# Optimization experiments

Measured on AMD Instinct MI355X. Metric: run time of the kernel, lower is better.

## Reference

```python
import jax, jax.numpy as jnp
import numpy as np

FEATURE_DIM = 64
HIDDEN = 128

def _xavier(key, shape):
    fan_in, fan_out = shape
    limit = float(np.sqrt(6.0 / (fan_in + fan_out)))
    return jax.random.uniform(key, shape, jnp.float32, -limit, limit)

def setup_inputs() -> dict:
    key = jax.random.key(0)
    ks = jax.random.split(key, 12)
    x = jax.random.normal(ks[0], (64, 4096, FEATURE_DIM), jnp.float32)
    h_t = jax.random.normal(ks[1], (64 * 4096, HIDDEN), jnp.float32)
    c_t = jax.random.normal(ks[2], (64 * 4096, HIDDEN), jnp.float32)
    W_xi = _xavier(ks[3], (FEATURE_DIM, HIDDEN)); W_hi = _xavier(ks[4], (HIDDEN, HIDDEN))
    W_xf = _xavier(ks[5], (FEATURE_DIM, HIDDEN)); W_hf = _xavier(ks[6], (HIDDEN, HIDDEN))
    W_xc = _xavier(ks[7], (FEATURE_DIM, HIDDEN)); W_hc = _xavier(ks[8], (HIDDEN, HIDDEN))
    W_xo = _xavier(ks[9], (FEATURE_DIM, HIDDEN)); W_ho = _xavier(ks[10], (HIDDEN, HIDDEN))
    b_i = jnp.zeros((HIDDEN,), jnp.float32)
    b_f = jnp.zeros((HIDDEN,), jnp.float32)
    b_c = jnp.zeros((HIDDEN,), jnp.float32)
    b_o = jnp.zeros((HIDDEN,), jnp.float32)
    return {"x": x, "h_t": h_t, "c_t": c_t,
            "W_xi": W_xi, "W_hi": W_hi, "b_i": b_i,
            "W_xf": W_xf, "W_hf": W_hf, "b_f": b_f,
            "W_xc": W_xc, "W_hc": W_hc, "b_c": b_c,
            "W_xo": W_xo, "W_ho": W_ho, "b_o": b_o}

def reference(x, h_t, c_t, W_xi, W_hi, b_i, W_xf, W_hf, b_f, W_xc, W_hc, b_c, W_xo, W_ho, b_o):
    bs, num_nodes, feature_dim = x.shape
    xf = x.reshape(bs * num_nodes, feature_dim)  # [N, F]
    # Fused form: concatenate the 4 gate weights -> 2 GEMMs + one elementwise pass
    Wx = jnp.concatenate([W_xi, W_xf, W_xc, W_xo], axis=1)   # [F, 4H]
    Wh = jnp.concatenate([W_hi, W_hf, W_hc, W_ho], axis=1)   # [H, 4H]
    b = jnp.concatenate([b_i, b_f, b_c, b_o])                # [4H]
    gates = xf @ Wx + h_t @ Wh + b                           # [N, 4H]
    H = h_t.shape[1]
    i_t = jax.nn.sigmoid(gates[:, 0 * H:1 * H])
    f_t = jax.nn.sigmoid(gates[:, 1 * H:2 * H])
    c_hat = jnp.tanh(gates[:, 2 * H:3 * H])
    o_t = jax.nn.sigmoid(gates[:, 3 * H:4 * H])
    c_new = f_t * c_t + i_t * c_hat
    h_new = o_t * jnp.tanh(c_new)
    return (h_new, c_new)
```

## Files before the change

### kernel.cpp

```cpp
#include <hip/hip_runtime.h>
#include <hip/hip_bf16.h>


#define N_ROWS (64 * 4096)
#define HDIM 128
#define FDIM 64
#define KDIM 192
#define NKS 12
#define M_TILE 32

typedef __bf16 bf16_t;
typedef __bf16 bf16x8 __attribute__((ext_vector_type(8)));
typedef float f32x16 __attribute__((ext_vector_type(16)));

__global__ void swizzle_weights(const float* __restrict__ Wxi, const float* __restrict__ Whi,
                                const float* __restrict__ Wxf, const float* __restrict__ Whf,
                                const float* __restrict__ Wxc, const float* __restrict__ Whc,
                                const float* __restrict__ Wxo, const float* __restrict__ Who,
                                bf16_t* __restrict__ Bsw) {
    int gid = blockIdx.x * 256 + threadIdx.x;
    int l  = gid & 63;
    int ct = (gid >> 6) & 15;
    int ks = gid >> 10;
    int kb = ks * 16 + (l >> 5) * 8;
    int n  = ct * 32 + (l & 31);
    int g  = n >> 7;
    int c  = n & 127;
    const float* Wx = (g == 0) ? Wxi : (g == 1) ? Wxf : (g == 2) ? Wxc : Wxo;
    const float* Wh = (g == 0) ? Whi : (g == 1) ? Whf : (g == 2) ? Whc : Who;
    bf16x8 v;
#pragma unroll
    for (int j = 0; j < 8; ++j) {
        int k = kb + j;
        float f = (k < FDIM) ? Wx[k * HDIM + c] : Wh[(k - FDIM) * HDIM + c];
        v[j] = (bf16_t)f;
    }
    *(bf16x8*)(Bsw + (long)gid * 8) = v;
}

__device__ inline float fast_rcp(float x) { return __builtin_amdgcn_rcpf(x); }
__device__ inline float sigm(float x) {
    x = fminf(fmaxf(x, -30.f), 30.f);
    return fast_rcp(1.f + __expf(-x));
}
__device__ inline float tanh_f(float x) {
    x = fminf(fmaxf(x, -15.f), 15.f);
    float e = __expf(-2.f * x);
    return (1.f - e) * fast_rcp(1.f + e);
}

__global__ __launch_bounds__(256, 3)
void lstm_fused(const float* __restrict__ x, const float* __restrict__ h_t,
                const float* __restrict__ c_t,
                const float* __restrict__ b_i, const float* __restrict__ b_f,
                const float* __restrict__ b_c, const float* __restrict__ b_o,
                const bf16_t* __restrict__ Bsw,
                float* __restrict__ h_out, float* __restrict__ c_out) {
    const int tid  = threadIdx.x;
    const int wave = tid >> 6;
    const int lane = tid & 63;
    const long row_base = (long)blockIdx.x * M_TILE;

    const int arow = lane & 31;
    const int ksl  = (lane >> 5) * 8;
    const float* ax = x   + (row_base + arow) * FDIM + ksl;
    const float* ah = h_t + (row_base + arow) * HDIM + ksl;

    const int col   = wave * 32 + (lane & 31);
    const int rhalf = 4 * (lane >> 5);

    float cpre[16];
#pragma unroll
    for (int r = 0; r < 16; ++r) {
        int row_l = (r & 3) + 8 * (r >> 2) + rhalf;
        cpre[r] = c_t[(row_base + row_l) * HDIM + col];
    }
    const float bi = b_i[col], bf = b_f[col], bc = b_c[col], bo = b_o[col];

    f32x16 acc0 = {}, acc1 = {}, acc2 = {}, acc3 = {};
    const bf16_t* b_base = Bsw + wave * 512 + (long)lane * 8;

#pragma unroll
    for (int ks = 0; ks < NKS; ++ks) {
        const float* ap = (ks < 4) ? (ax + ks * 16) : (ah + (ks - 4) * 16);
        float4 f0 = *(const float4*)(ap);
        float4 f1 = *(const float4*)(ap + 4);
        bf16x8 a;
        a[0] = (bf16_t)f0.x; a[1] = (bf16_t)f0.y; a[2] = (bf16_t)f0.z; a[3] = (bf16_t)f0.w;
        a[4] = (bf16_t)f1.x; a[5] = (bf16_t)f1.y; a[6] = (bf16_t)f1.z; a[7] = (bf16_t)f1.w;

        const bf16_t* bp = b_base + (long)ks * 8192;
        bf16x8 b0 = *(const bf16x8*)(bp);
        bf16x8 b1 = *(const bf16x8*)(bp + 2048);
        bf16x8 b2 = *(const bf16x8*)(bp + 4096);
        bf16x8 b3 = *(const bf16x8*)(bp + 6144);
        acc0 = __builtin_amdgcn_mfma_f32_32x32x16_bf16(a, b0, acc0, 0, 0, 0);
        acc1 = __builtin_amdgcn_mfma_f32_32x32x16_bf16(a, b1, acc1, 0, 0, 0);
        acc2 = __builtin_amdgcn_mfma_f32_32x32x16_bf16(a, b2, acc2, 0, 0, 0);
        acc3 = __builtin_amdgcn_mfma_f32_32x32x16_bf16(a, b3, acc3, 0, 0, 0);
    }

#pragma unroll
    for (int r = 0; r < 16; ++r) {
        int row_l = (r & 3) + 8 * (r >> 2) + rhalf;
        long idx = (row_base + row_l) * HDIM + col;
        float gi = acc0[r] + bi;
        float gf = acc1[r] + bf;
        float gc = acc2[r] + bc;
        float go = acc3[r] + bo;
        float i_t = sigm(gi);
        float f_t = sigm(gf);
        float ch  = tanh_f(gc);
        float o_t = sigm(go);
        float cn = f_t * cpre[r] + i_t * ch;
        float hn = o_t * tanh_f(cn);
        h_out[idx] = hn;
        c_out[idx] = cn;
    }
}

extern "C" void kernel_launch(void* const* d_in, const int* in_sizes, int n_in,
                              void* d_out, int out_size, void* d_ws, size_t ws_size,
                              hipStream_t stream) {
    const float* x    = (const float*)d_in[0];
    const float* h_t  = (const float*)d_in[1];
    const float* c_t  = (const float*)d_in[2];
    const float* W_xi = (const float*)d_in[3];
    const float* W_hi = (const float*)d_in[4];
    const float* b_i  = (const float*)d_in[5];
    const float* W_xf = (const float*)d_in[6];
    const float* W_hf = (const float*)d_in[7];
    const float* b_f  = (const float*)d_in[8];
    const float* W_xc = (const float*)d_in[9];
    const float* W_hc = (const float*)d_in[10];
    const float* b_c  = (const float*)d_in[11];
    const float* W_xo = (const float*)d_in[12];
    const float* W_ho = (const float*)d_in[13];
    const float* b_o  = (const float*)d_in[14];

    bf16_t* Bsw = (bf16_t*)d_ws;
    float* h_out = (float*)d_out;
    float* c_out = h_out + (long)N_ROWS * HDIM;

    swizzle_weights<<<48, 256, 0, stream>>>(W_xi, W_hi, W_xf, W_hf,
                                            W_xc, W_hc, W_xo, W_ho, Bsw);
    lstm_fused<<<N_ROWS / M_TILE, 256, 0, stream>>>(x, h_t, c_t, b_i, b_f, b_c, b_o,
                                                    Bsw, h_out, c_out);
}
```

Baseline: 616.0 us.

## Retile LSTM kernel by row block and gate column, staging weights in LDS

```diff
diff --git a/kernel.cpp b/kernel.cpp
--- a/kernel.cpp
+++ b/kernel.cpp
@@ -7,7 +7,8 @@
 #define FDIM 64
 #define KDIM 192
 #define NKS 12
-#define M_TILE 32
+#define RBLK 128
+#define PH_KS 6
 
 typedef __bf16 bf16_t;
 typedef __bf16 bf16x8 __attribute__((ext_vector_type(8)));
@@ -49,61 +50,85 @@
     return (1.f - e) * fast_rcp(1.f + e);
 }
 
-__global__ __launch_bounds__(256, 3)
+__global__ __launch_bounds__(256, 4)
 void lstm_fused(const float* __restrict__ x, const float* __restrict__ h_t,
                 const float* __restrict__ c_t,
                 const float* __restrict__ b_i, const float* __restrict__ b_f,
                 const float* __restrict__ b_c, const float* __restrict__ b_o,
                 const bf16_t* __restrict__ Bsw,
                 float* __restrict__ h_out, float* __restrict__ c_out) {
+    __shared__ bf16_t bsh[PH_KS * 4 * 512];
+
     const int tid  = threadIdx.x;
     const int wave = tid >> 6;
     const int lane = tid & 63;
-    const long row_base = (long)blockIdx.x * M_TILE;
 
-    const int arow = lane & 31;
-    const int ksl  = (lane >> 5) * 8;
-    const float* ax = x   + (row_base + arow) * FDIM + ksl;
-    const float* ah = h_t + (row_base + arow) * HDIM + ksl;
+    const int bid     = blockIdx.x;
+    const int logical = ((bid & 7) << 10) | (bid >> 3);
+    const int c_blk   = logical & 3;
+    const long row_base = (long)(logical >> 2) * RBLK;
 
-    const int col   = wave * 32 + (lane & 31);
+    const int r0  = wave * 32 + (lane & 31);
+    const int ksl = (lane >> 5) * 8;
+    const float* ax = x   + (row_base + r0) * FDIM + ksl;
+    const float* ah = h_t + (row_base + r0) * HDIM + ksl;
+
+    const int col   = c_blk * 32 + (lane & 31);
     const int rhalf = 4 * (lane >> 5);
+    const int wrow  = wave * 32;
 
     float cpre[16];
 #pragma unroll
     for (int r = 0; r < 16; ++r) {
         int row_l = (r & 3) + 8 * (r >> 2) + rhalf;
-        cpre[r] = c_t[(row_base + row_l) * HDIM + col];
+        cpre[r] = c_t[(row_base + wrow + row_l) * HDIM + col];
     }
     const float bi = b_i[col], bf = b_f[col], bc = b_c[col], bo = b_o[col];
 
     f32x16 acc0 = {}, acc1 = {}, acc2 = {}, acc3 = {};
-    const bf16_t* b_base = Bsw + wave * 512 + (long)lane * 8;
 
 #pragma unroll
-    for (int ks = 0; ks < NKS; ++ks) {
-        const float* ap = (ks < 4) ? (ax + ks * 16) : (ah + (ks - 4) * 16);
-        float4 f0 = *(const float4*)(ap);
-        float4 f1 = *(const float4*)(ap + 4);
-        bf16x8 a;
-        a[0] = (bf16_t)f0.x; a[1] = (bf16_t)f0.y; a[2] = (bf16_t)f0.z; a[3] = (bf16_t)f0.w;
-        a[4] = (bf16_t)f1.x; a[5] = (bf16_t)f1.y; a[6] = (bf16_t)f1.z; a[7] = (bf16_t)f1.w;
+    for (int ph = 0; ph < 2; ++ph) {
+        if (ph) __syncthreads();
+#pragma unroll
+        for (int i = 0; i < PH_KS; ++i) {
+            int q   = wave * PH_KS + i;
+            int ks6 = q >> 2, g = q & 3;
+            const bf16_t* src = Bsw + ((long)((ph * PH_KS + ks6) * 16 + g * 4 + c_blk) << 9)
+                                    + lane * 8;
+            bf16_t* dst = bsh + q * 512;
+            __builtin_amdgcn_global_load_lds(
+                (const __attribute__((address_space(1))) unsigned int*)src,
+                (__attribute__((address_space(3))) unsigned int*)dst, 16, 0, 0);
+        }
+        __syncthreads();
 
-        const bf16_t* bp = b_base + (long)ks * 8192;
-        bf16x8 b0 = *(const bf16x8*)(bp);
-        bf16x8 b1 = *(const bf16x8*)(bp + 2048);
-        bf16x8 b2 = *(const bf16x8*)(bp + 4096);
-        bf16x8 b3 = *(const bf16x8*)(bp + 6144);
-        acc0 = __builtin_amdgcn_mfma_f32_32x32x16_bf16(a, b0, acc0, 0, 0, 0);
-        acc1 = __builtin_amdgcn_mfma_f32_32x32x16_bf16(a, b1, acc1, 0, 0, 0);
-        acc2 = __builtin_amdgcn_mfma_f32_32x32x16_bf16(a, b2, acc2, 0, 0, 0);
-        acc3 = __builtin_amdgcn_mfma_f32_32x32x16_bf16(a, b3, acc3, 0, 0, 0);
+#pragma unroll
+        for (int ks6 = 0; ks6 < PH_KS; ++ks6) {
+            int ksg = ph * PH_KS + ks6;
+            const float* ap = (ksg < 4) ? (ax + ksg * 16) : (ah + (ksg - 4) * 16);
+            float4 f0 = *(const float4*)(ap);
+            float4 f1 = *(const float4*)(ap + 4);
+            bf16x8 a;
+            a[0] = (bf16_t)f0.x; a[1] = (bf16_t)f0.y; a[2] = (bf16_t)f0.z; a[3] = (bf16_t)f0.w;
+            a[4] = (bf16_t)f1.x; a[5] = (bf16_t)f1.y; a[6] = (bf16_t)f1.z; a[7] = (bf16_t)f1.w;
+
+            const bf16_t* bp = bsh + (ks6 * 4) * 512 + lane * 8;
+            bf16x8 b0 = *(const bf16x8*)(bp);
+            bf16x8 b1 = *(const bf16x8*)(bp + 512);
+            bf16x8 b2 = *(const bf16x8*)(bp + 1024);
+            bf16x8 b3 = *(const bf16x8*)(bp + 1536);
+            acc0 = __builtin_amdgcn_mfma_f32_32x32x16_bf16(a, b0, acc0, 0, 0, 0);
+            acc1 = __builtin_amdgcn_mfma_f32_32x32x16_bf16(a, b1, acc1, 0, 0, 0);
+            acc2 = __builtin_amdgcn_mfma_f32_32x32x16_bf16(a, b2, acc2, 0, 0, 0);
+            acc3 = __builtin_amdgcn_mfma_f32_32x32x16_bf16(a, b3, acc3, 0, 0, 0);
+        }
     }
 
 #pragma unroll
     for (int r = 0; r < 16; ++r) {
         int row_l = (r & 3) + 8 * (r >> 2) + rhalf;
-        long idx = (row_base + row_l) * HDIM + col;
+        long idx = (row_base + wrow + row_l) * HDIM + col;
         float gi = acc0[r] + bi;
         float gf = acc1[r] + bf;
         float gc = acc2[r] + bc;
@@ -144,6 +169,6 @@
 
     swizzle_weights<<<48, 256, 0, stream>>>(W_xi, W_hi, W_xf, W_hf,
                                             W_xc, W_hc, W_xo, W_ho, Bsw);
-    lstm_fused<<<N_ROWS / M_TILE, 256, 0, stream>>>(x, h_t, c_t, b_i, b_f, b_c, b_o,
-                                                    Bsw, h_out, c_out);
+    lstm_fused<<<(N_ROWS / RBLK) * 4, 256, 0, stream>>>(x, h_t, c_t, b_i, b_f, b_c, b_o,
+                                                        Bsw, h_out, c_out);
 }
```

Result: slower. 663.0 us (+7.6%).

## Keep weights in registers across persistent row tiles using 16x16x32 MFMA

Applied to the files above, without the earlier changes.

```diff
diff --git a/kernel.cpp b/kernel.cpp
--- a/kernel.cpp
+++ b/kernel.cpp
@@ -5,27 +5,27 @@
 #define N_ROWS (64 * 4096)
 #define HDIM 128
 #define FDIM 64
-#define KDIM 192
-#define NKS 12
-#define M_TILE 32
+#define RPT 16
+#define TILES 8
 
 typedef __bf16 bf16_t;
 typedef __bf16 bf16x8 __attribute__((ext_vector_type(8)));
-typedef float f32x16 __attribute__((ext_vector_type(16)));
+typedef float f32x4 __attribute__((ext_vector_type(4)));
+
+#define MFMA16(a, b, c) __builtin_amdgcn_mfma_f32_16x16x32_bf16(a, b, c, 0, 0, 0)
 
 __global__ void swizzle_weights(const float* __restrict__ Wxi, const float* __restrict__ Whi,
                                 const float* __restrict__ Wxf, const float* __restrict__ Whf,
                                 const float* __restrict__ Wxc, const float* __restrict__ Whc,
                                 const float* __restrict__ Wxo, const float* __restrict__ Who,
                                 bf16_t* __restrict__ Bsw) {
-    int gid = blockIdx.x * 256 + threadIdx.x;
-    int l  = gid & 63;
-    int ct = (gid >> 6) & 15;
-    int ks = gid >> 10;
-    int kb = ks * 16 + (l >> 5) * 8;
-    int n  = ct * 32 + (l & 31);
-    int g  = n >> 7;
-    int c  = n & 127;
+    int gid  = blockIdx.x * 256 + threadIdx.x;
+    int lane = gid & 63;
+    int w    = (gid >> 6) & 7;
+    int g    = (gid >> 9) & 3;
+    int ks   = gid >> 11;
+    int kb   = ks * 32 + ((lane >> 4) & 3) * 8;
+    int c    = w * 16 + (lane & 15);
     const float* Wx = (g == 0) ? Wxi : (g == 1) ? Wxf : (g == 2) ? Wxc : Wxo;
     const float* Wh = (g == 0) ? Whi : (g == 1) ? Whf : (g == 2) ? Whc : Who;
     bf16x8 v;
@@ -39,17 +39,17 @@
 }
 
 __device__ inline float fast_rcp(float x) { return __builtin_amdgcn_rcpf(x); }
-__device__ inline float sigm(float x) {
-    x = fminf(fmaxf(x, -30.f), 30.f);
-    return fast_rcp(1.f + __expf(-x));
-}
-__device__ inline float tanh_f(float x) {
-    x = fminf(fmaxf(x, -15.f), 15.f);
-    float e = __expf(-2.f * x);
-    return (1.f - e) * fast_rcp(1.f + e);
+__device__ inline float sigm(float x) { return fast_rcp(1.f + __expf(-x)); }
+__device__ inline float tanh_f(float x) { return 1.f - 2.f * fast_rcp(1.f + __expf(2.f * x)); }
+
+__device__ inline bf16x8 cvt8(float4 a, float4 b) {
+    bf16x8 r;
+    r[0] = (bf16_t)a.x; r[1] = (bf16_t)a.y; r[2] = (bf16_t)a.z; r[3] = (bf16_t)a.w;
+    r[4] = (bf16_t)b.x; r[5] = (bf16_t)b.y; r[6] = (bf16_t)b.z; r[7] = (bf16_t)b.w;
+    return r;
 }
 
-__global__ __launch_bounds__(256, 3)
+__global__ __launch_bounds__(512, 2)
 void lstm_fused(const float* __restrict__ x, const float* __restrict__ h_t,
                 const float* __restrict__ c_t,
                 const float* __restrict__ b_i, const float* __restrict__ b_f,
@@ -57,65 +57,84 @@
                 const bf16_t* __restrict__ Bsw,
                 float* __restrict__ h_out, float* __restrict__ c_out) {
     const int tid  = threadIdx.x;
-    const int wave = tid >> 6;
+    const int wv   = tid >> 6;
     const int lane = tid & 63;
-    const long row_base = (long)blockIdx.x * M_TILE;
+    const long row0 = (long)blockIdx.x * (RPT * TILES);
 
-    const int arow = lane & 31;
-    const int ksl  = (lane >> 5) * 8;
-    const float* ax = x   + (row_base + arow) * FDIM + ksl;
-    const float* ah = h_t + (row_base + arow) * HDIM + ksl;
+    const int arow = lane & 15;
+    const int kof  = (lane >> 4) * 8;
 
-    const int col   = wave * 32 + (lane & 31);
-    const int rhalf = 4 * (lane >> 5);
+    bf16x8 breg[24];
+#pragma unroll
+    for (int ks = 0; ks < 6; ++ks)
+#pragma unroll
+        for (int g = 0; g < 4; ++g)
+            breg[ks * 4 + g] =
+                *(const bf16x8*)(Bsw + ((long)((ks * 4 + g) * 8 + wv) << 9) + lane * 8);
 
-    float cpre[16];
+    const int col  = wv * 16 + (lane & 15);
+    const int orow = (lane >> 4) * 4;
+    const float bi = b_i[col], bff = b_f[col], bcc = b_c[col], boo = b_o[col];
+
+    for (int t = 0; t < TILES; ++t) {
+        const long rb = row0 + (long)t * RPT;
+        const float* xr = x   + (rb + arow) * FDIM + kof;
+        const float* hr = h_t + (rb + arow) * HDIM + kof;
+
+        float4 x0 = *(const float4*)(xr);
+        float4 x1 = *(const float4*)(xr + 4);
+        float4 x2 = *(const float4*)(xr + 32);
+        float4 x3 = *(const float4*)(xr + 36);
+        float4 h0 = *(const float4*)(hr);
+        float4 h1 = *(const float4*)(hr + 4);
+        float cp[4];
 #pragma unroll
-    for (int r = 0; r < 16; ++r) {
-        int row_l = (r & 3) + 8 * (r >> 2) + rhalf;
-        cpre[r] = c_t[(row_base + row_l) * HDIM + col];
-    }
-    const float bi = b_i[col], bf = b_f[col], bc = b_c[col], bo = b_o[col];
+        for (int r = 0; r < 4; ++r)
+            cp[r] = c_t[(rb + orow + r) * HDIM + col];
+        float4 h2 = *(const float4*)(hr + 32);
+        float4 h3 = *(const float4*)(hr + 36);
+        float4 h4 = *(const float4*)(hr + 64);
+        float4 h5 = *(const float4*)(hr + 68);
+        float4 h6 = *(const float4*)(hr + 96);
+        float4 h7 = *(const float4*)(hr + 100);
 
-    f32x16 acc0 = {}, acc1 = {}, acc2 = {}, acc3 = {};
-    const bf16_t* b_base = Bsw + wave * 512 + (long)lane * 8;
+        f32x4 acc0 = {}, acc1 = {}, acc2 = {}, acc3 = {};
+        bf16x8 a;
+        a = cvt8(x0, x1);
+        acc0 = MFMA16(a, breg[0],  acc0); acc1 = MFMA16(a, breg[1],  acc1);
+        acc2 = MFMA16(a, breg[2],  acc2); acc3 = MFMA16(a, breg[3],  acc3);
+        a = cvt8(x2, x3);
+        acc0 = MFMA16(a, breg[4],  acc0); acc1 = MFMA16(a, breg[5],  acc1);
+        acc2 = MFMA16(a, breg[6],  acc2); acc3 = MFMA16(a, breg[7],  acc3);
+        a = cvt8(h0, h1);
+        acc0 = MFMA16(a, breg[8],  acc0); acc1 = MFMA16(a, breg[9],  acc1);
+        acc2 = MFMA16(a, breg[10], acc2); acc3 = MFMA16(a, breg[11], acc3);
+        a = cvt8(h2, h3);
+        acc0 = MFMA16(a, breg[12], acc0); acc1 = MFMA16(a, breg[13], acc1);
+        acc2 = MFMA16(a, breg[14], acc2); acc3 = MFMA16(a, breg[15], acc3);
+        a = cvt8(h4, h5);
+        acc0 = MFMA16(a, breg[16], acc0); acc1 = MFMA16(a, breg[17], acc1);
+        acc2 = MFMA16(a, breg[18], acc2); acc3 = MFMA16(a, breg[19], acc3);
+        a = cvt8(h6, h7);
+        acc0 = MFMA16(a, breg[20], acc0); acc1 = MFMA16(a, breg[21], acc1);
+        acc2 = MFMA16(a, breg[22], acc2); acc3 = MFMA16(a, breg[23], acc3);
 
 #pragma unroll
-    for (int ks = 0; ks < NKS; ++ks) {
-        const float* ap = (ks < 4) ? (ax + ks * 16) : (ah + (ks - 4) * 16);
-        float4 f0 = *(const float4*)(ap);
-        float4 f1 = *(const float4*)(ap + 4);
-        bf16x8 a;
-        a[0] = (bf16_t)f0.x; a[1] = (bf16_t)f0.y; a[2] = (bf16_t)f0.z; a[3] = (bf16_t)f0.w;
-        a[4] = (bf16_t)f1.x; a[5] = (bf16_t)f1.y; a[6] = (bf16_t)f1.z; a[7] = (bf16_t)f1.w;
-
-        const bf16_t* bp = b_base + (long)ks * 8192;
-        bf16x8 b0 = *(const bf16x8*)(bp);
-        bf16x8 b1 = *(const bf16x8*)(bp + 2048);
-        bf16x8 b2 = *(const bf16x8*)(bp + 4096);
-        bf16x8 b3 = *(const bf16x8*)(bp + 6144);
-        acc0 = __builtin_amdgcn_mfma_f32_32x32x16_bf16(a, b0, acc0, 0, 0, 0);
-        acc1 = __builtin_amdgcn_mfma_f32_32x32x16_bf16(a, b1, acc1, 0, 0, 0);
-        acc2 = __builtin_amdgcn_mfma_f32_32x32x16_bf16(a, b2, acc2, 0, 0, 0);
-        acc3 = __builtin_amdgcn_mfma_f32_32x32x16_bf16(a, b3, acc3, 0, 0, 0);
-    }
-
-#pragma unroll
-    for (int r = 0; r < 16; ++r) {
-        int row_l = (r & 3) + 8 * (r >> 2) + rhalf;
-        long idx = (row_base + row_l) * HDIM + col;
-        float gi = acc0[r] + bi;
-        float gf = acc1[r] + bf;
-        float gc = acc2[r] + bc;
-        float go = acc3[r] + bo;
-        float i_t = sigm(gi);
-        float f_t = sigm(gf);
-        float ch  = tanh_f(gc);
-        float o_t = sigm(go);
-        float cn = f_t * cpre[r] + i_t * ch;
-        float hn = o_t * tanh_f(cn);
-        h_out[idx] = hn;
-        c_out[idx] = cn;
+        for (int r = 0; r < 4; ++r) {
+            long idx = (rb + orow + r) * HDIM + col;
+            float gi = acc0[r] + bi;
+            float gf = acc1[r] + bff;
+            float gc = acc2[r] + bcc;
+            float go = acc3[r] + boo;
+            float i_t = sigm(gi);
+            float f_t = sigm(gf);
+            float ch  = tanh_f(gc);
+            float o_t = sigm(go);
+            float cn = f_t * cp[r] + i_t * ch;
+            float hn = o_t * tanh_f(cn);
+            h_out[idx] = hn;
+            c_out[idx] = cn;
+        }
     }
 }
 
@@ -144,6 +163,7 @@
 
     swizzle_weights<<<48, 256, 0, stream>>>(W_xi, W_hi, W_xf, W_hf,
                                             W_xc, W_hc, W_xo, W_ho, Bsw);
-    lstm_fused<<<N_ROWS / M_TILE, 256, 0, stream>>>(x, h_t, c_t, b_i, b_f, b_c, b_o,
-                                                    Bsw, h_out, c_out);
+    lstm_fused<<<N_ROWS / (RPT * TILES), 512, 0, stream>>>(x, h_t, c_t,
+                                                           b_i, b_f, b_c, b_o,
+                                                           Bsw, h_out, c_out);
 }
```

Result: slower. 646.7 us (+5.0%).
